# Optimization experiments

Hardware: AMD Instinct MI355X
Metric: run time of the kernel (lower is better)

The kernel has to match this reference:

```python
import jax, jax.numpy as jnp
import numpy as np

DIM_K = 32


def setup_inputs() -> dict:
    N, DORI, DAPP, DK, NCLS = 4096, 2048, 512, 32, 21
    key = jax.random.key(0)
    ks = jax.random.split(key, 16)
    std = 0.01
    inp = {
        'rois': jax.random.normal(ks[0], (N, 5), jnp.float32),
        'delta_rois': jax.random.normal(ks[1], (9, N, 5), jnp.float32),
        'features': jax.random.normal(ks[2], (9, N, DORI), jnp.float32),
        'gt_features': jax.random.normal(ks[3], (1, N, DORI), jnp.float32),
        'ious': jax.random.uniform(ks[4], (9, 1, N), jnp.float32),
        # learned parameters (singleton broadcast dims squeezed out)
        'attention_feat': jax.random.normal(ks[5], (DORI, DAPP), jnp.float32) * std,
        'w_k': jax.random.normal(ks[6], (DAPP, DK, 4), jnp.float32) * std,
        'w_q': jax.random.normal(ks[7], (9, DAPP, DK, 4), jnp.float32) * std,
        'alpha_w': jax.random.normal(ks[8], (9, DORI, 4), jnp.float32) * std,
        'bbox_regress': jax.random.normal(ks[9], (9, DORI, 4), jnp.float32) * 0.001,
        'w_k_cls': jax.random.normal(ks[10], (DAPP, DK, 1), jnp.float32) * std,
        'w_q_cls': jax.random.normal(ks[11], (9, DAPP, DK, 1), jnp.float32) * std,
        'alpha_w_cls': jax.random.normal(ks[12], (9, DORI, 1), jnp.float32) * std,
        'cls_score_w': jax.random.normal(ks[13], (9, DORI, NCLS), jnp.float32) * std,
    }
    return inp


def reference(rois, delta_rois, features, gt_features, ious,
              attention_feat, w_k, w_q, alpha_w, bbox_regress,
              w_k_cls, w_q_cls, alpha_w_cls, cls_score_w):
    # features: (9, N, DORI). The torch code materializes (9,N,DORI,DAPP)
    # via broadcast-mul + sum; einsum computes the identical contraction.
    off = jax.nn.relu(jnp.einsum('anf,fd->and', features, attention_feat))  # (9,N,DAPP)

    alpha = jnp.einsum('anf,afc->anc', features, alpha_w)          # (9,N,4)
    offset = jnp.einsum('anf,afc->anc', features, bbox_regress)   # (9,N,4)
    alpha_softmax = jax.nn.softmax(alpha, axis=0)
    delta8 = delta_rois[:, :, 1:5]                                  # (9,N,4)
    delta_pred_offset = delta8 + offset
    output = jnp.sum(delta_pred_offset * alpha_softmax, axis=0)    # (N,4)

    # ---- classification branch ----
    cls_score = jnp.einsum('anf,afc->anc', features, cls_score_w)  # (9,N,NCLS)
    alpha_cls = jnp.einsum('anf,afc->anc', features, alpha_w_cls)  # (9,N,1)
    alpha_softmax_cls = jax.nn.softmax(alpha_cls, axis=0)

    # ---- training-only beta (query/key) attention ----
    query_out = jnp.einsum('and,adkc->ankc', off, w_q)          # (9,N,DK,4)
    query_out_cls = jnp.einsum('and,adkc->ankc', off, w_q_cls)  # (9,N,DK,1)
    gt_off = jax.nn.relu(jnp.einsum('nf,fd->nd', gt_features[0], attention_feat))  # (N,DAPP)
    key_out = jnp.einsum('nd,dkc->nkc', gt_off, w_k)            # (N,DK,4)
    key_out_cls = jnp.einsum('nd,dkc->nkc', gt_off, w_k_cls)    # (N,DK,1)

    scale = 1.0 / np.sqrt(DIM_K).astype(np.float32)
    beta_out = jnp.einsum('ankc,nkc->anc', query_out, key_out) * scale - ious[:, 0, :, None]  # (9,N,4)
    beta_softmax = jax.nn.softmax(beta_out, axis=0)
    beta_out_cls = jnp.einsum('ankc,nkc->anc', query_out_cls, key_out_cls) * scale - ious.reshape(9, -1, 1)  # (9,N,1)
    beta_softmax_cls = jax.nn.softmax(beta_out_cls, axis=0)

    output_beta = jnp.sum(delta_pred_offset * beta_softmax, axis=0)  # (N,4)

    return (output, output_beta, alpha_softmax, beta_softmax,
            delta_pred_offset, delta_pred_offset, alpha, beta_out,
            cls_score, alpha_softmax_cls, beta_softmax_cls, alpha_cls, beta_out_cls)
```

## Files before the change

### kernel.cpp

```cpp
#include <hip/hip_runtime.h>

using u16 = unsigned short;
using s16x8 = __attribute__((ext_vector_type(8))) short;
using f32x4 = __attribute__((ext_vector_type(4))) float;

#define DEVI __device__ __forceinline__

constexpr int AN = 9, NB = 10, NN = 4096, DORI = 2048, DAPP = 512, NCLS = 21, QCOLS = 160;

constexpr size_t O0 = 0;
constexpr size_t O1 = 16384;
constexpr size_t O2 = 32768;
constexpr size_t O3 = 180224;
constexpr size_t O4 = 327680;
constexpr size_t O5 = 475136;
constexpr size_t O6 = 622592;
constexpr size_t O7 = 770048;
constexpr size_t O8 = 917504;
constexpr size_t O9 = 1691648;
constexpr size_t O10 = 1728512;
constexpr size_t O11 = 1765376;
constexpr size_t O12 = 1802240;

DEVI u16 f2b(float f) {
  unsigned u = __float_as_uint(f);
  unsigned r = (u + 0x7fffu + ((u >> 16) & 1u)) >> 16;
  return (u16)r;
}

DEVI uint4 pack8(float4 u, float4 v) {
  uint4 r;
  r.x = (unsigned)f2b(u.x) | ((unsigned)f2b(u.y) << 16);
  r.y = (unsigned)f2b(u.z) | ((unsigned)f2b(u.w) << 16);
  r.z = (unsigned)f2b(v.x) | ((unsigned)f2b(v.y) << 16);
  r.w = (unsigned)f2b(v.z) | ((unsigned)f2b(v.w) << 16);
  return r;
}

DEVI void gload_lds16(const u16* g, u16* l) {
  __builtin_amdgcn_global_load_lds(
      (const __attribute__((address_space(1))) void*)g,
      (__attribute__((address_space(3))) void*)l, 16, 0, 0);
}

__global__ __launch_bounds__(256) void prep(const float* __restrict__ att,
                                            const float* __restrict__ wq,
                                            const float* __restrict__ wqc,
                                            const float* __restrict__ wk,
                                            const float* __restrict__ wkc,
                                            const float* __restrict__ aw,
                                            const float* __restrict__ bb,
                                            const float* __restrict__ awc,
                                            const float* __restrict__ cw,
                                            const float* __restrict__ gt,
                                            u16* __restrict__ attB,
                                            u16* __restrict__ Wq,
                                            u16* __restrict__ Wsm,
                                            u16* __restrict__ featB9) {
  const int b = blockIdx.x, tid = threadIdx.x;
  if (b < 4096) {
    int t = b * 256 + tid;
    int c = t / DORI, d = t % DORI;
    attB[t] = f2b(att[(size_t)d * DAPP + c]);
  } else if (b < 7296) {
    int t = (b - 4096) * 256 + tid;
    int bq = t / (QCOLS * DAPP);
    int r = t % (QCOLS * DAPP);
    int col = r / DAPP, d = r % DAPP;
    float v;
    if (bq < 9) {
      if (col < 128) v = wq[(size_t)bq * DAPP * 128 + (size_t)d * 128 + col];
      else           v = wqc[(size_t)bq * DAPP * 32 + (size_t)d * 32 + (col - 128)];
    } else {
      if (col < 128) v = wk[(size_t)d * 128 + col];
      else           v = wkc[(size_t)d * 32 + (col - 128)];
    }
    Wq[t] = f2b(v);
  } else if (b < 7368) {
    int t = (b - 7296) * 256 + tid;
    if (t >= AN * DORI) return;
    int a = t / DORI, f = t % DORI;
    u16* Wa = Wsm + (size_t)a * 32 * DORI;
    for (int c = 0; c < 4; ++c)  Wa[c * DORI + f]       = f2b(aw[((size_t)a * DORI + f) * 4 + c]);
    for (int c = 0; c < 4; ++c)  Wa[(4 + c) * DORI + f] = f2b(bb[((size_t)a * DORI + f) * 4 + c]);
    for (int c = 0; c < 21; ++c) Wa[(8 + c) * DORI + f] = f2b(cw[((size_t)a * DORI + f) * 21 + c]);
    Wa[29 * DORI + f] = f2b(awc[(size_t)a * DORI + f]);
    Wa[30 * DORI + f] = 0;
    Wa[31 * DORI + f] = 0;
  } else {
    if (!featB9) return;
    long i = (long)(b - 7368) * 256 + tid;
    float4 v0 = ((const float4*)gt)[i * 2];
    float4 v1 = ((const float4*)gt)[i * 2 + 1];
    ((uint4*)featB9)[i] = pack8(v0, v1);
  }
}

__global__ __launch_bounds__(256) void feat_gemm(const float* __restrict__ feat,
                                                 const u16* __restrict__ Wsm,
                                                 float* __restrict__ smallf,
                                                 u16* __restrict__ wb,
                                                 float* __restrict__ cls_out) {
  __shared__ __align__(16) u16 As[64 * 32];
  __shared__ __align__(16) u16 Bs[32 * 32];
  const int tid = threadIdx.x, lane = tid & 63, wave = tid >> 6;
  const int tileM = blockIdx.y * 64, batch = blockIdx.z;
  const float* Ab = feat + ((size_t)batch * NN + tileM) * DORI;
  const u16* Bb = Wsm + (size_t)batch * 32 * DORI;
  u16* wbp = wb ? wb + ((size_t)batch * NN + tileM) * DORI : nullptr;

  f32x4 acc0 = {0.f, 0.f, 0.f, 0.f}, acc1 = {0.f, 0.f, 0.f, 0.f};
  const int arow = tid >> 2, acol = (tid & 3) * 8;
  const bool bact = tid < 128;

  uint4 raA, rbA, raB, rbB;
  auto loadA = [&](int k0) {
    const float* s = Ab + (size_t)arow * DORI + k0 + acol;
    raA = pack8(*(const float4*)s, *(const float4*)(s + 4));
    if (bact) rbA = *(const uint4*)(Bb + (size_t)arow * DORI + k0 + acol);
  };
  auto loadB = [&](int k0) {
    const float* s = Ab + (size_t)arow * DORI + k0 + acol;
    raB = pack8(*(const float4*)s, *(const float4*)(s + 4));
    if (bact) rbB = *(const uint4*)(Bb + (size_t)arow * DORI + k0 + acol);
  };
  loadA(0);
  loadB(32);
  const u16* Arow = As + (wave * 16 + (lane & 15)) * 32 + (lane >> 4) * 8;
  const u16* Brow = Bs + (lane & 15) * 32 + (lane >> 4) * 8;

  for (int k0 = 0; k0 < DORI; k0 += 64) {
    __syncthreads();
    *(uint4*)(As + (size_t)tid * 8) = raA;
    if (bact) *(uint4*)(Bs + (size_t)tid * 8) = rbA;
    if (wbp) *(uint4*)(wbp + (size_t)arow * DORI + k0 + acol) = raA;
    __syncthreads();
    if (k0 + 64 < DORI) loadA(k0 + 64);
    {
      s16x8 af = *(const s16x8*)Arow;
      s16x8 b0 = *(const s16x8*)Brow;
      s16x8 b1 = *(const s16x8*)(Brow + 16 * 32);
      acc0 = __builtin_amdgcn_mfma_f32_16x16x32_bf16(af, b0, acc0, 0, 0, 0);
      acc1 = __builtin_amdgcn_mfma_f32_16x16x32_bf16(af, b1, acc1, 0, 0, 0);
    }
    __syncthreads();
    *(uint4*)(As + (size_t)tid * 8) = raB;
    if (bact) *(uint4*)(Bs + (size_t)tid * 8) = rbB;
    if (wbp) *(uint4*)(wbp + (size_t)arow * DORI + k0 + 32 + acol) = raB;
    __syncthreads();
    if (k0 + 96 < DORI) loadB(k0 + 96);
    {
      s16x8 af = *(const s16x8*)Arow;
      s16x8 b0 = *(const s16x8*)Brow;
      s16x8 b1 = *(const s16x8*)(Brow + 16 * 32);
      acc0 = __builtin_amdgcn_mfma_f32_16x16x32_bf16(af, b0, acc0, 0, 0, 0);
      acc1 = __builtin_amdgcn_mfma_f32_16x16x32_bf16(af, b1, acc1, 0, 0, 0);
    }
  }

  const int r0 = tileM + wave * 16 + (lane >> 4) * 4;
  const int c0 = lane & 15;
#pragma unroll
  for (int q = 0; q < 4; ++q) {
    const size_t an = (size_t)batch * NN + r0 + q;
    smallf[an * 32 + c0]      = acc0[q];
    smallf[an * 32 + c0 + 16] = acc1[q];
    if (c0 >= 8)  cls_out[an * 21 + (c0 - 8)] = acc0[q];
    if (c0 <= 12) cls_out[an * 21 + (c0 + 8)] = acc1[q];
  }
}

template<int BM, int BN, int WM, int WN, bool RELU, bool OUTBF, bool SWZ>
__global__ __launch_bounds__(WM * WN * 64)
void gemm_glds(const u16* __restrict__ A, long sA, const u16* __restrict__ B, long sB,
               void* __restrict__ Cv, long sC, int N, int K) {
  constexpr int THREADS = WM * WN * 64;
  constexpr int WTM = BM / WM, WTN = BN / WN;
  constexpr int FM = WTM / 16, FN = WTN / 16;
  constexpr int ACHN = BM * 4, BCHN = BN * 4;
  constexpr int ACH = (ACHN + THREADS - 1) / THREADS;
  constexpr int BCH = (BCHN + THREADS - 1) / THREADS;
  constexpr bool AFULL = (ACHN % THREADS) == 0, BFULL = (BCHN % THREADS) == 0;

  __shared__ __align__(16) u16 As[BM * 32];
  __shared__ __align__(16) u16 Bs[BN * 32];

  int bx = blockIdx.x, by = blockIdx.y, bz = blockIdx.z;
  if constexpr (SWZ) {
    int gx = gridDim.x, gy = gridDim.y;
    int h = bx + gx * (by + gy * bz);
    int nwg = gx * gy * (int)gridDim.z;
    int cpx = nwg >> 3;
    int l = (h & 7) * cpx + (h >> 3);
    bx = l % gx; l /= gx; by = l % gy; bz = l / gy;
  }

  const int tid = threadIdx.x, lane = tid & 63, wave = tid >> 6;
  const int wm = wave % WM, wn = wave / WM;
  const int tileN = bx * BN, tileM = by * BM;
  const u16* Ab = A + (size_t)bz * sA + (size_t)tileM * K;
  const u16* Bb = B + (size_t)bz * sB + (size_t)tileN * K;

  f32x4 acc[FM][FN];
#pragma unroll
  for (int i = 0; i < FM; ++i)
#pragma unroll
    for (int j = 0; j < FN; ++j) acc[i][j] = (f32x4){0.f, 0.f, 0.f, 0.f};

  const u16* Arow = As + (wm * WTM + (lane & 15)) * 32 + (lane >> 4) * 8;
  const u16* Brow = Bs + (wn * WTN + (lane & 15)) * 32 + (lane >> 4) * 8;

  for (int k0 = 0; k0 < K; k0 += 32) {
#pragma unroll
    for (int i = 0; i < ACH; ++i) {
      int c = tid + i * THREADS;
      if (AFULL || c < ACHN)
        gload_lds16(Ab + (size_t)(c >> 2) * K + k0 + (c & 3) * 8, As + c * 8);
    }
#pragma unroll
    for (int i = 0; i < BCH; ++i) {
      int c = tid + i * THREADS;
      if (BFULL || c < BCHN)
        gload_lds16(Bb + (size_t)(c >> 2) * K + k0 + (c & 3) * 8, Bs + c * 8);
    }
    __syncthreads();
    s16x8 af[FM], bfr[FN];
#pragma unroll
    for (int i = 0; i < FM; ++i) af[i] = *(const s16x8*)(Arow + i * 16 * 32);
#pragma unroll
    for (int j = 0; j < FN; ++j) bfr[j] = *(const s16x8*)(Brow + j * 16 * 32);
#pragma unroll
    for (int i = 0; i < FM; ++i)
#pragma unroll
      for (int j = 0; j < FN; ++j)
        acc[i][j] = __builtin_amdgcn_mfma_f32_16x16x32_bf16(af[i], bfr[j], acc[i][j], 0, 0, 0);
    __syncthreads();
  }

  const int r0 = tileM + wm * WTM + (lane >> 4) * 4;
  const int c0 = tileN + wn * WTN + (lane & 15);
#pragma unroll
  for (int i = 0; i < FM; ++i)
#pragma unroll
    for (int j = 0; j < FN; ++j)
#pragma unroll
      for (int q = 0; q < 4; ++q) {
        float v = acc[i][j][q];
        if (RELU) v = fmaxf(v, 0.f);
        size_t idx = (size_t)bz * sC + (size_t)(r0 + i * 16 + q) * N + (c0 + j * 16);
        if (OUTBF) ((u16*)Cv)[idx] = f2b(v);
        else       ((float*)Cv)[idx] = v;
      }
}

template<int BM, int BN, int WM, int WN, bool RELU, bool OUTBF>
__global__ __launch_bounds__(WM * WN * 64)
void gemm_af32(const float* __restrict__ Av, const float* __restrict__ A2v, long sA,
               const u16* __restrict__ B, long sB,
               void* __restrict__ Cv, long sC, int N, int K) {
  constexpr int THREADS = WM * WN * 64;
  constexpr int WTM = BM / WM, WTN = BN / WN;
  constexpr int FM = WTM / 16, FN = WTN / 16;
  constexpr int ACH = (BM * 4) / THREADS;
  constexpr int BCHN = BN * 4;
  constexpr int BCH = (BCHN + THREADS - 1) / THREADS;
  constexpr bool BFULL = (BCHN % THREADS) == 0;

  __shared__ __align__(16) u16 As[BM * 32];
  __shared__ __align__(16) u16 Bs[BN * 32];

  const int tid = threadIdx.x, lane = tid & 63, wave = tid >> 6;
  const int wm = wave % WM, wn = wave / WM;
  const int tileN = blockIdx.x * BN, tileM = blockIdx.y * BM;
  const int batch = blockIdx.z;
  const float* base = (batch < 9) ? (Av + (size_t)batch * sA) : A2v;
  const float* Ab32 = base + (size_t)tileM * K;
  const u16* Bb = B + (size_t)batch * sB + (size_t)tileN * K;

  f32x4 acc[FM][FN];
#pragma unroll
  for (int i = 0; i < FM; ++i)
#pragma unroll
    for (int j = 0; j < FN; ++j) acc[i][j] = (f32x4){0.f, 0.f, 0.f, 0.f};

  uint4 ra[ACH], rb[BCH];
  auto load_t = [&](int k0) {
#pragma unroll
    for (int i = 0; i < ACH; ++i) {
      int c = tid + i * THREADS;
      const float* s = Ab32 + (size_t)(c >> 2) * K + k0 + (c & 3) * 8;
      ra[i] = pack8(*(const float4*)s, *(const float4*)(s + 4));
    }
#pragma unroll
    for (int i = 0; i < BCH; ++i) {
      int c = tid + i * THREADS;
      if (BFULL || c < BCHN)
        rb[i] = *(const uint4*)(Bb + (size_t)(c >> 2) * K + k0 + (c & 3) * 8);
    }
  };

  load_t(0);
  const u16* Arow = As + (wm * WTM + (lane & 15)) * 32 + (lane >> 4) * 8;
  const u16* Brow = Bs + (wn * WTN + (lane & 15)) * 32 + (lane >> 4) * 8;

  for (int k0 = 0; k0 < K; k0 += 32) {
    __syncthreads();
#pragma unroll
    for (int i = 0; i < ACH; ++i)
      *(uint4*)(As + (size_t)(tid + i * THREADS) * 8) = ra[i];
#pragma unroll
    for (int i = 0; i < BCH; ++i) {
      int c = tid + i * THREADS;
      if (BFULL || c < BCHN) *(uint4*)(Bs + (size_t)c * 8) = rb[i];
    }
    __syncthreads();
    if (k0 + 32 < K) load_t(k0 + 32);
    s16x8 af[FM], bfr[FN];
#pragma unroll
    for (int i = 0; i < FM; ++i) af[i] = *(const s16x8*)(Arow + i * 16 * 32);
#pragma unroll
    for (int j = 0; j < FN; ++j) bfr[j] = *(const s16x8*)(Brow + j * 16 * 32);
#pragma unroll
    for (int i = 0; i < FM; ++i)
#pragma unroll
      for (int j = 0; j < FN; ++j)
        acc[i][j] = __builtin_amdgcn_mfma_f32_16x16x32_bf16(af[i], bfr[j], acc[i][j], 0, 0, 0);
  }

  const int r0 = tileM + wm * WTM + (lane >> 4) * 4;
  const int c0 = tileN + wn * WTN + (lane & 15);
#pragma unroll
  for (int i = 0; i < FM; ++i)
#pragma unroll
    for (int j = 0; j < FN; ++j)
#pragma unroll
      for (int q = 0; q < 4; ++q) {
        float v = acc[i][j][q];
        if (RELU) v = fmaxf(v, 0.f);
        size_t idx = (size_t)batch * sC + (size_t)(r0 + i * 16 + q) * N + (c0 + j * 16);
        if (OUTBF) ((u16*)Cv)[idx] = f2b(v);
        else       ((float*)Cv)[idx] = v;
      }
}

__global__ __launch_bounds__(256) void gemm2qb(const u16* __restrict__ offb,
                                               const u16* __restrict__ Wq,
                                               const float* __restrict__ keyf,
                                               const float* __restrict__ ious,
                                               float* __restrict__ betaf,
                                               float* __restrict__ betac) {
  constexpr int BM = 128, BN = 160;
  __shared__ __align__(16) u16 As[BM * 32];
  __shared__ __align__(16) u16 Bs[BN * 32];
  const int tid = threadIdx.x, lane = tid & 63, wave = tid >> 6;
  const int tileM = blockIdx.x * BM;
  const int a = blockIdx.y;
  const u16* Ab = offb + ((size_t)a * NN + tileM) * DAPP;
  const u16* Bb = Wq + (size_t)a * QCOLS * DAPP;

  f32x4 acc[2][10];
#pragma unroll
  for (int i = 0; i < 2; ++i)
#pragma unroll
    for (int j = 0; j < 10; ++j) acc[i][j] = (f32x4){0.f, 0.f, 0.f, 0.f};

  const u16* Arow = As + (wave * 32 + (lane & 15)) * 32 + (lane >> 4) * 8;
  const u16* Brow = Bs + (lane & 15) * 32 + (lane >> 4) * 8;

  for (int k0 = 0; k0 < DAPP; k0 += 32) {
#pragma unroll
    for (int i = 0; i < 2; ++i) {
      int c = tid + i * 256;
      gload_lds16(Ab + (size_t)(c >> 2) * DAPP + k0 + (c & 3) * 8, As + c * 8);
    }
#pragma unroll
    for (int i = 0; i < 3; ++i) {
      int c = tid + i * 256;
      if (c < 640)
        gload_lds16(Bb + (size_t)(c >> 2) * DAPP + k0 + (c & 3) * 8, Bs + c * 8);
    }
    __syncthreads();
    s16x8 af[2], bfr[10];
#pragma unroll
    for (int i = 0; i < 2; ++i) af[i] = *(const s16x8*)(Arow + i * 16 * 32);
#pragma unroll
    for (int j = 0; j < 10; ++j) bfr[j] = *(const s16x8*)(Brow + j * 16 * 32);
#pragma unroll
    for (int i = 0; i < 2; ++i)
#pragma unroll
      for (int j = 0; j < 10; ++j)
        acc[i][j] = __builtin_amdgcn_mfma_f32_16x16x32_bf16(af[i], bfr[j], acc[i][j], 0, 0, 0);
    __syncthreads();
  }

  const float scale = 0.17677669529663687f;
  const int cg = lane & 15;
#pragma unroll
  for (int i = 0; i < 2; ++i)
#pragma unroll
    for (int q = 0; q < 4; ++q) {
      const int row = tileM + wave * 32 + i * 16 + (lane >> 4) * 4 + q;
      const float* kr = keyf + (size_t)row * QCOLS;
      float m = 0.f;
#pragma unroll
      for (int j = 0; j < 8; ++j) m += acc[i][j][q] * kr[cg + j * 16];
      float cl = acc[i][8][q] * kr[128 + cg] + acc[i][9][q] * kr[144 + cg];
      m += __shfl_xor(m, 4); m += __shfl_xor(m, 8);
      cl += __shfl_xor(cl, 1); cl += __shfl_xor(cl, 2);
      cl += __shfl_xor(cl, 4); cl += __shfl_xor(cl, 8);
      const float iou = ious[(size_t)a * NN + row];
      if (cg < 4)  betaf[((size_t)a * NN + row) * 4 + (lane & 3)] = m * scale - iou;
      if (cg == 0) betac[(size_t)a * NN + row] = cl * scale - iou;
    }
}

__global__ __launch_bounds__(256) void finalize(const float* __restrict__ smallf,
                                                const float* __restrict__ beta_ws,
                                                const float* __restrict__ betac_ws,
                                                const float* __restrict__ delta_rois,
                                                float* __restrict__ out) {
  int n = blockIdx.x * blockDim.x + threadIdx.x;
  if (n >= NN) return;

  for (int c = 0; c < 4; ++c) {
    float al[9], be[9], dp[9];
    float mA = -1e30f, mB = -1e30f;
    for (int a = 0; a < 9; ++a) {
      size_t an = (size_t)a * NN + n;
      al[a] = smallf[an * 32 + c];
      float off_ = smallf[an * 32 + 4 + c];
      dp[a] = delta_rois[an * 5 + 1 + c] + off_;
      be[a] = beta_ws[an * 4 + c];
      mA = fmaxf(mA, al[a]); mB = fmaxf(mB, be[a]);
    }
    float eA[9], eB[9], sA = 0.f, sB = 0.f;
    for (int a = 0; a < 9; ++a) {
      eA[a] = expf(al[a] - mA); sA += eA[a];
      eB[a] = expf(be[a] - mB); sB += eB[a];
    }
    float rA = 1.f / sA, rB = 1.f / sB;
    float ov = 0.f, obv = 0.f;
    for (int a = 0; a < 9; ++a) {
      size_t an = (size_t)a * NN + n;
      float as_ = eA[a] * rA, bs_ = eB[a] * rB;
      out[O2 + an * 4 + c] = as_;
      out[O3 + an * 4 + c] = bs_;
      out[O4 + an * 4 + c] = dp[a];
      out[O5 + an * 4 + c] = dp[a];
      out[O6 + an * 4 + c] = al[a];
      out[O7 + an * 4 + c] = be[a];
      ov += dp[a] * as_; obv += dp[a] * bs_;
    }
    out[O0 + (size_t)n * 4 + c] = ov;
    out[O1 + (size_t)n * 4 + c] = obv;
  }

  float ac[9], bc[9];
  float mA = -1e30f, mB = -1e30f;
  for (int a = 0; a < 9; ++a) {
    size_t an = (size_t)a * NN + n;
    ac[a] = smallf[an * 32 + 29];
    bc[a] = betac_ws[an];
    mA = fmaxf(mA, ac[a]); mB = fmaxf(mB, bc[a]);
  }
  float eA[9], eB[9], sA = 0.f, sB = 0.f;
  for (int a = 0; a < 9; ++a) {
    eA[a] = expf(ac[a] - mA); sA += eA[a];
    eB[a] = expf(bc[a] - mB); sB += eB[a];
  }
  float rA = 1.f / sA, rB = 1.f / sB;
  for (int a = 0; a < 9; ++a) {
    size_t an = (size_t)a * NN + n;
    out[O9 + an]  = eA[a] * rA;
    out[O10 + an] = eB[a] * rB;
    out[O11 + an] = ac[a];
    out[O12 + an] = bc[a];
  }
}

extern "C" void kernel_launch(void* const* d_in, const int* in_sizes, int n_in,
                              void* d_out, int out_size, void* d_ws, size_t ws_size,
                              hipStream_t stream) {
  const float* delta_rois = (const float*)d_in[1];
  const float* features   = (const float*)d_in[2];
  const float* gt_features= (const float*)d_in[3];
  const float* ious       = (const float*)d_in[4];
  const float* att        = (const float*)d_in[5];
  const float* w_k        = (const float*)d_in[6];
  const float* w_q        = (const float*)d_in[7];
  const float* alpha_w    = (const float*)d_in[8];
  const float* bbox       = (const float*)d_in[9];
  const float* w_k_cls    = (const float*)d_in[10];
  const float* w_q_cls    = (const float*)d_in[11];
  const float* alpha_w_cls= (const float*)d_in[12];
  const float* cls_w      = (const float*)d_in[13];
  float* out = (float*)d_out;

  char* ws = (char*)d_ws;
  u16* attB    = (u16*)ws;   ws += (size_t)DAPP * DORI * 2;
  u16* Wq      = (u16*)ws;   ws += (size_t)NB * QCOLS * DAPP * 2;
  u16* Wsmall  = (u16*)ws;   ws += (size_t)AN * 32 * DORI * 2;
  u16* offb    = (u16*)ws;   ws += (size_t)NB * NN * DAPP * 2;
  float* smallf= (float*)ws; ws += (size_t)AN * NN * 32 * 4;
  float* keyf  = (float*)ws; ws += (size_t)NN * QCOLS * 4;
  float* betaf = (float*)ws; ws += (size_t)AN * NN * 4 * 4;
  float* betac = (float*)ws; ws += (size_t)AN * NN * 4;
  size_t base_bytes = (size_t)(ws - (char*)d_ws);
  size_t featB_bytes = (size_t)NB * NN * DORI * 2;
  bool big = ws_size >= base_bytes + featB_bytes;
  u16* featB = big ? (u16*)ws : nullptr;

  prep<<<11464, 256, 0, stream>>>(att, w_q, w_q_cls, w_k, w_k_cls, alpha_w, bbox,
                                  alpha_w_cls, cls_w, gt_features, attB, Wq, Wsmall,
                                  big ? featB + (size_t)AN * NN * DORI : nullptr);

  dim3 gf(1, NN / 64, AN);
  feat_gemm<<<gf, 256, 0, stream>>>(features, Wsmall, smallf, featB, out + O8);

  dim3 g1(DAPP / 128, NN / 128, NB);
  if (big) {
    gemm_glds<128, 128, 2, 2, true, true, true><<<g1, 256, 0, stream>>>(
        featB, (long)NN * DORI, attB, 0, offb, (long)NN * DAPP, DAPP, DORI);
  } else {
    gemm_af32<128, 128, 2, 2, true, true><<<g1, 256, 0, stream>>>(
        features, gt_features, (long)NN * DORI, attB, 0, offb, (long)NN * DAPP, DAPP, DORI);
  }

  dim3 gk(QCOLS / 32, NN / 128, 1);
  gemm_glds<128, 32, 4, 1, false, false, false><<<gk, 256, 0, stream>>>(
      offb + (size_t)9 * NN * DAPP, 0, Wq + (size_t)9 * QCOLS * DAPP, 0,
      keyf, 0, QCOLS, DAPP);

  dim3 g2(NN / 128, AN, 1);
  gemm2qb<<<g2, 256, 0, stream>>>(offb, Wq, keyf, ious, betaf, betac);

  finalize<<<NN / 256, 256, 0, stream>>>(smallf, betaf, betac, delta_rois, out);
}
```

Before: 340.1 us.

## Fuse small-weight GEMM and attention-feature GEMM into one kernel reading fp32 features once

Replaces the separate feat_gemm (which wrote a bf16 copy of features) and the big feature×attention GEMM with a single 512-thread kernel. Each block loads a 64-row fp32 feature tile once, converts it to bf16, and multiplies it against all 512 attention columns plus the 32 small-weight columns. The aim is to avoid writing and re-reading a bf16 copy of the features and to drop a launch. In exchange the M tile is only 64 rows, the grid is small at 640 blocks, the B tile in LDS is large, and the k-loop has no LDS double buffering.

```diff
diff --git a/kernel.cpp b/kernel.cpp
--- a/kernel.cpp
+++ b/kernel.cpp
@@ -52,11 +52,9 @@
                                             const float* __restrict__ bb,
                                             const float* __restrict__ awc,
                                             const float* __restrict__ cw,
-                                            const float* __restrict__ gt,
                                             u16* __restrict__ attB,
                                             u16* __restrict__ Wq,
-                                            u16* __restrict__ Wsm,
-                                            u16* __restrict__ featB9) {
+                                            u16* __restrict__ Wsm) {
   const int b = blockIdx.x, tid = threadIdx.x;
   if (b < 4096) {
     int t = b * 256 + tid;
@@ -76,7 +74,7 @@
       else           v = wkc[(size_t)d * 32 + (col - 128)];
     }
     Wq[t] = f2b(v);
-  } else if (b < 7368) {
+  } else {
     int t = (b - 7296) * 256 + tid;
     if (t >= AN * DORI) return;
     int a = t / DORI, f = t % DORI;
@@ -87,86 +85,110 @@
     Wa[29 * DORI + f] = f2b(awc[(size_t)a * DORI + f]);
     Wa[30 * DORI + f] = 0;
     Wa[31 * DORI + f] = 0;
-  } else {
-    if (!featB9) return;
-    long i = (long)(b - 7368) * 256 + tid;
-    float4 v0 = ((const float4*)gt)[i * 2];
-    float4 v1 = ((const float4*)gt)[i * 2 + 1];
-    ((uint4*)featB9)[i] = pack8(v0, v1);
-  }
-}
-
-__global__ __launch_bounds__(256) void feat_gemm(const float* __restrict__ feat,
-                                                 const u16* __restrict__ Wsm,
-                                                 float* __restrict__ smallf,
-                                                 u16* __restrict__ wb,
-                                                 float* __restrict__ cls_out) {
+  }
+}
+
+__global__ __launch_bounds__(512) void mega(const float* __restrict__ feat,
+                                            const float* __restrict__ gt,
+                                            const u16* __restrict__ attB,
+                                            const u16* __restrict__ Wsm,
+                                            u16* __restrict__ offb,
+                                            float* __restrict__ smallf,
+                                            float* __restrict__ cls_out) {
   __shared__ __align__(16) u16 As[64 * 32];
-  __shared__ __align__(16) u16 Bs[32 * 32];
-  const int tid = threadIdx.x, lane = tid & 63, wave = tid >> 6;
-  const int tileM = blockIdx.y * 64, batch = blockIdx.z;
-  const float* Ab = feat + ((size_t)batch * NN + tileM) * DORI;
-  const u16* Bb = Wsm + (size_t)batch * 32 * DORI;
-  u16* wbp = wb ? wb + ((size_t)batch * NN + tileM) * DORI : nullptr;
-
-  f32x4 acc0 = {0.f, 0.f, 0.f, 0.f}, acc1 = {0.f, 0.f, 0.f, 0.f};
+  __shared__ __align__(16) u16 Bs[544 * 32];
+  const int tid = threadIdx.x, lane = tid & 63, w = tid >> 6;
+  const int tileM = blockIdx.y * 64, z = blockIdx.z;
+  const float* Ab = ((z < 9) ? feat + (size_t)z * NN * DORI : gt) + (size_t)tileM * DORI;
+  const u16* Wb = Wsm + (size_t)((z < 9) ? z : 0) * 32 * DORI;
+
+  f32x4 acc[4][4], accS[4];
+#pragma unroll
+  for (int i = 0; i < 4; ++i) {
+#pragma unroll
+    for (int j = 0; j < 4; ++j) acc[i][j] = (f32x4){0.f, 0.f, 0.f, 0.f};
+    accS[i] = (f32x4){0.f, 0.f, 0.f, 0.f};
+  }
+
   const int arow = tid >> 2, acol = (tid & 3) * 8;
-  const bool bact = tid < 128;
-
-  uint4 raA, rbA, raB, rbB;
-  auto loadA = [&](int k0) {
+  const bool aact = tid < 256;
+  uint4 raA, raB;
+  auto loadA = [&](int k0, uint4& r) {
     const float* s = Ab + (size_t)arow * DORI + k0 + acol;
-    raA = pack8(*(const float4*)s, *(const float4*)(s + 4));
-    if (bact) rbA = *(const uint4*)(Bb + (size_t)arow * DORI + k0 + acol);
+    r = pack8(*(const float4*)s, *(const float4*)(s + 4));
   };
-  auto loadB = [&](int k0) {
-    const float* s = Ab + (size_t)arow * DORI + k0 + acol;
-    raB = pack8(*(const float4*)s, *(const float4*)(s + 4));
-    if (bact) rbB = *(const uint4*)(Bb + (size_t)arow * DORI + k0 + acol);
+  if (aact) { loadA(0, raA); loadA(32, raB); }
+
+  auto stageB = [&](int k0) {
+#pragma unroll
+    for (int i = 0; i < 4; ++i) {
+      int c = tid + i * 512;
+      gload_lds16(attB + (size_t)(c >> 2) * DORI + k0 + (c & 3) * 8, Bs + c * 8);
+    }
+    if (tid < 128) {
+      int c = 2048 + tid;
+      gload_lds16(Wb + (size_t)((c >> 2) - 512) * DORI + k0 + (c & 3) * 8, Bs + c * 8);
+    }
   };
-  loadA(0);
-  loadB(32);
-  const u16* Arow = As + (wave * 16 + (lane & 15)) * 32 + (lane >> 4) * 8;
-  const u16* Brow = Bs + (lane & 15) * 32 + (lane >> 4) * 8;
+
+  const u16* Arow = As + (lane & 15) * 32 + (lane >> 4) * 8;
+  const u16* Brow = Bs + (w * 64 + (lane & 15)) * 32 + (lane >> 4) * 8;
+  const u16* BrowS = Bs + (512 + w * 16 + (lane & 15)) * 32 + (lane >> 4) * 8;
+
+  auto step = [&](int k0, uint4 ra) {
+    if (aact) *(uint4*)(As + (size_t)tid * 8) = ra;
+    stageB(k0);
+    __syncthreads();
+    s16x8 af[4], bfr[4];
+#pragma unroll
+    for (int i = 0; i < 4; ++i) af[i] = *(const s16x8*)(Arow + i * 16 * 32);
+#pragma unroll
+    for (int j = 0; j < 4; ++j) bfr[j] = *(const s16x8*)(Brow + j * 16 * 32);
+#pragma unroll
+    for (int i = 0; i < 4; ++i)
+#pragma unroll
+      for (int j = 0; j < 4; ++j)
+        acc[i][j] = __builtin_amdgcn_mfma_f32_16x16x32_bf16(af[i], bfr[j], acc[i][j], 0, 0, 0);
+    if (w < 2) {
+      s16x8 bs = *(const s16x8*)BrowS;
+#pragma unroll
+      for (int i = 0; i < 4; ++i)
+        accS[i] = __builtin_amdgcn_mfma_f32_16x16x32_bf16(af[i], bs, accS[i], 0, 0, 0);
+    }
+    __syncthreads();
+  };
 
   for (int k0 = 0; k0 < DORI; k0 += 64) {
-    __syncthreads();
-    *(uint4*)(As + (size_t)tid * 8) = raA;
-    if (bact) *(uint4*)(Bs + (size_t)tid * 8) = rbA;
-    if (wbp) *(uint4*)(wbp + (size_t)arow * DORI + k0 + acol) = raA;
-    __syncthreads();
-    if (k0 + 64 < DORI) loadA(k0 + 64);
-    {
-      s16x8 af = *(const s16x8*)Arow;
-      s16x8 b0 = *(const s16x8*)Brow;
-      s16x8 b1 = *(const s16x8*)(Brow + 16 * 32);
-      acc0 = __builtin_amdgcn_mfma_f32_16x16x32_bf16(af, b0, acc0, 0, 0, 0);
-      acc1 = __builtin_amdgcn_mfma_f32_16x16x32_bf16(af, b1, acc1, 0, 0, 0);
-    }
-    __syncthreads();
-    *(uint4*)(As + (size_t)tid * 8) = raB;
-    if (bact) *(uint4*)(Bs + (size_t)tid * 8) = rbB;
-    if (wbp) *(uint4*)(wbp + (size_t)arow * DORI + k0 + 32 + acol) = raB;
-    __syncthreads();
-    if (k0 + 96 < DORI) loadB(k0 + 96);
-    {
-      s16x8 af = *(const s16x8*)Arow;
-      s16x8 b0 = *(const s16x8*)Brow;
-      s16x8 b1 = *(const s16x8*)(Brow + 16 * 32);
-      acc0 = __builtin_amdgcn_mfma_f32_16x16x32_bf16(af, b0, acc0, 0, 0, 0);
-      acc1 = __builtin_amdgcn_mfma_f32_16x16x32_bf16(af, b1, acc1, 0, 0, 0);
-    }
-  }
-
-  const int r0 = tileM + wave * 16 + (lane >> 4) * 4;
-  const int c0 = lane & 15;
-#pragma unroll
-  for (int q = 0; q < 4; ++q) {
-    const size_t an = (size_t)batch * NN + r0 + q;
-    smallf[an * 32 + c0]      = acc0[q];
-    smallf[an * 32 + c0 + 16] = acc1[q];
-    if (c0 >= 8)  cls_out[an * 21 + (c0 - 8)] = acc0[q];
-    if (c0 <= 12) cls_out[an * 21 + (c0 + 8)] = acc1[q];
+    uint4 curA = raA, curB = raB;
+    if (aact && k0 + 64 < DORI) loadA(k0 + 64, raA);
+    step(k0, curA);
+    if (aact && k0 + 96 < DORI) loadA(k0 + 96, raB);
+    step(k0 + 32, curB);
+  }
+
+#pragma unroll
+  for (int i = 0; i < 4; ++i) {
+    const int row = tileM + i * 16 + (lane >> 4) * 4;
+    const int col = w * 64 + (lane & 15);
+#pragma unroll
+    for (int j = 0; j < 4; ++j)
+#pragma unroll
+      for (int q = 0; q < 4; ++q)
+        offb[((size_t)z * NN + row + q) * DAPP + col + j * 16] =
+            f2b(fmaxf(acc[i][j][q], 0.f));
+  }
+  if (w < 2 && z < 9) {
+    const int cs = w * 16 + (lane & 15);
+#pragma unroll
+    for (int i = 0; i < 4; ++i) {
+      const int row = tileM + i * 16 + (lane >> 4) * 4;
+#pragma unroll
+      for (int q = 0; q < 4; ++q) {
+        const size_t an = (size_t)z * NN + row + q;
+        smallf[an * 32 + cs] = accS[i][q];
+        if (cs >= 8 && cs <= 28) cls_out[an * 21 + (cs - 8)] = accS[i][q];
+      }
+    }
   }
 }
 
@@ -248,96 +270,6 @@
         float v = acc[i][j][q];
         if (RELU) v = fmaxf(v, 0.f);
         size_t idx = (size_t)bz * sC + (size_t)(r0 + i * 16 + q) * N + (c0 + j * 16);
-        if (OUTBF) ((u16*)Cv)[idx] = f2b(v);
-        else       ((float*)Cv)[idx] = v;
-      }
-}
-
-template<int BM, int BN, int WM, int WN, bool RELU, bool OUTBF>
-__global__ __launch_bounds__(WM * WN * 64)
-void gemm_af32(const float* __restrict__ Av, const float* __restrict__ A2v, long sA,
-               const u16* __restrict__ B, long sB,
-               void* __restrict__ Cv, long sC, int N, int K) {
-  constexpr int THREADS = WM * WN * 64;
-  constexpr int WTM = BM / WM, WTN = BN / WN;
-  constexpr int FM = WTM / 16, FN = WTN / 16;
-  constexpr int ACH = (BM * 4) / THREADS;
-  constexpr int BCHN = BN * 4;
-  constexpr int BCH = (BCHN + THREADS - 1) / THREADS;
-  constexpr bool BFULL = (BCHN % THREADS) == 0;
-
-  __shared__ __align__(16) u16 As[BM * 32];
-  __shared__ __align__(16) u16 Bs[BN * 32];
-
-  const int tid = threadIdx.x, lane = tid & 63, wave = tid >> 6;
-  const int wm = wave % WM, wn = wave / WM;
-  const int tileN = blockIdx.x * BN, tileM = blockIdx.y * BM;
-  const int batch = blockIdx.z;
-  const float* base = (batch < 9) ? (Av + (size_t)batch * sA) : A2v;
-  const float* Ab32 = base + (size_t)tileM * K;
-  const u16* Bb = B + (size_t)batch * sB + (size_t)tileN * K;
-
-  f32x4 acc[FM][FN];
-#pragma unroll
-  for (int i = 0; i < FM; ++i)
-#pragma unroll
-    for (int j = 0; j < FN; ++j) acc[i][j] = (f32x4){0.f, 0.f, 0.f, 0.f};
-
-  uint4 ra[ACH], rb[BCH];
-  auto load_t = [&](int k0) {
-#pragma unroll
-    for (int i = 0; i < ACH; ++i) {
-      int c = tid + i * THREADS;
-      const float* s = Ab32 + (size_t)(c >> 2) * K + k0 + (c & 3) * 8;
-      ra[i] = pack8(*(const float4*)s, *(const float4*)(s + 4));
-    }
-#pragma unroll
-    for (int i = 0; i < BCH; ++i) {
-      int c = tid + i * THREADS;
-      if (BFULL || c < BCHN)
-        rb[i] = *(const uint4*)(Bb + (size_t)(c >> 2) * K + k0 + (c & 3) * 8);
-    }
-  };
-
-  load_t(0);
-  const u16* Arow = As + (wm * WTM + (lane & 15)) * 32 + (lane >> 4) * 8;
-  const u16* Brow = Bs + (wn * WTN + (lane & 15)) * 32 + (lane >> 4) * 8;
-
-  for (int k0 = 0; k0 < K; k0 += 32) {
-    __syncthreads();
-#pragma unroll
-    for (int i = 0; i < ACH; ++i)
-      *(uint4*)(As + (size_t)(tid + i * THREADS) * 8) = ra[i];
-#pragma unroll
-    for (int i = 0; i < BCH; ++i) {
-      int c = tid + i * THREADS;
-      if (BFULL || c < BCHN) *(uint4*)(Bs + (size_t)c * 8) = rb[i];
-    }
-    __syncthreads();
-    if (k0 + 32 < K) load_t(k0 + 32);
-    s16x8 af[FM], bfr[FN];
-#pragma unroll
-    for (int i = 0; i < FM; ++i) af[i] = *(const s16x8*)(Arow + i * 16 * 32);
-#pragma unroll
-    for (int j = 0; j < FN; ++j) bfr[j] = *(const s16x8*)(Brow + j * 16 * 32);
-#pragma unroll
-    for (int i = 0; i < FM; ++i)
-#pragma unroll
-      for (int j = 0; j < FN; ++j)
-        acc[i][j] = __builtin_amdgcn_mfma_f32_16x16x32_bf16(af[i], bfr[j], acc[i][j], 0, 0, 0);
-  }
-
-  const int r0 = tileM + wm * WTM + (lane >> 4) * 4;
-  const int c0 = tileN + wn * WTN + (lane & 15);
-#pragma unroll
-  for (int i = 0; i < FM; ++i)
-#pragma unroll
-    for (int j = 0; j < FN; ++j)
-#pragma unroll
-      for (int q = 0; q < 4; ++q) {
-        float v = acc[i][j][q];
-        if (RELU) v = fmaxf(v, 0.f);
-        size_t idx = (size_t)batch * sC + (size_t)(r0 + i * 16 + q) * N + (c0 + j * 16);
         if (OUTBF) ((u16*)Cv)[idx] = f2b(v);
         else       ((float*)Cv)[idx] = v;
       }
@@ -505,26 +437,13 @@
   float* keyf  = (float*)ws; ws += (size_t)NN * QCOLS * 4;
   float* betaf = (float*)ws; ws += (size_t)AN * NN * 4 * 4;
   float* betac = (float*)ws; ws += (size_t)AN * NN * 4;
-  size_t base_bytes = (size_t)(ws - (char*)d_ws);
-  size_t featB_bytes = (size_t)NB * NN * DORI * 2;
-  bool big = ws_size >= base_bytes + featB_bytes;
-  u16* featB = big ? (u16*)ws : nullptr;
-
-  prep<<<11464, 256, 0, stream>>>(att, w_q, w_q_cls, w_k, w_k_cls, alpha_w, bbox,
-                                  alpha_w_cls, cls_w, gt_features, attB, Wq, Wsmall,
-                                  big ? featB + (size_t)AN * NN * DORI : nullptr);
-
-  dim3 gf(1, NN / 64, AN);
-  feat_gemm<<<gf, 256, 0, stream>>>(features, Wsmall, smallf, featB, out + O8);
-
-  dim3 g1(DAPP / 128, NN / 128, NB);
-  if (big) {
-    gemm_glds<128, 128, 2, 2, true, true, true><<<g1, 256, 0, stream>>>(
-        featB, (long)NN * DORI, attB, 0, offb, (long)NN * DAPP, DAPP, DORI);
-  } else {
-    gemm_af32<128, 128, 2, 2, true, true><<<g1, 256, 0, stream>>>(
-        features, gt_features, (long)NN * DORI, attB, 0, offb, (long)NN * DAPP, DAPP, DORI);
-  }
+
+  prep<<<7368, 256, 0, stream>>>(att, w_q, w_q_cls, w_k, w_k_cls, alpha_w, bbox,
+                                 alpha_w_cls, cls_w, attB, Wq, Wsmall);
+
+  dim3 gm(1, NN / 64, NB);
+  mega<<<gm, 512, 0, stream>>>(features, gt_features, attB, Wsmall,
+                               offb, smallf, out + O8);
 
   dim3 gk(QCOLS / 32, NN / 128, 1);
   gemm_glds<128, 32, 4, 1, false, false, false><<<gk, 256, 0, stream>>>(
```

Result: slower. 358.6 us (+5.5%).

## Split fused feature cast+small GEMM into standalone cast and LDS-direct small GEMM

Applied to the files above, without the earlier changes.

Replaces the feat_gemm kernel, which converted fp32 features to bf16 while also writing the bf16 copy and computing the small alpha/offset/cls projections, with a separate grid-stride cast kernel and a new gemm_small kernel. gemm_small reads the bf16 copy through global_load_lds with 128-row tiles. The aim is to stop the small, MFMA-light GEMM from being bound by the fp32 loads and conversion. In exchange the bf16 features (about 150MB) are re-read once more. The fallback path now uses gemm_af32 plus a cls_copy kernel.

```diff
diff --git a/kernel.cpp b/kernel.cpp
--- a/kernel.cpp
+++ b/kernel.cpp
@@ -41,6 +41,17 @@
   __builtin_amdgcn_global_load_lds(
       (const __attribute__((address_space(1))) void*)g,
       (__attribute__((address_space(3))) void*)l, 16, 0, 0);
+}
+
+__global__ __launch_bounds__(256) void cast_kernel(const float* __restrict__ src,
+                                                   u16* __restrict__ dst, long n8) {
+  long i = (long)blockIdx.x * blockDim.x + threadIdx.x;
+  long stride = (long)gridDim.x * blockDim.x;
+  for (; i < n8; i += stride) {
+    float4 v0 = ((const float4*)src)[i * 2];
+    float4 v1 = ((const float4*)src)[i * 2 + 1];
+    ((uint4*)dst)[i] = pack8(v0, v1);
+  }
 }
 
 __global__ __launch_bounds__(256) void prep(const float* __restrict__ att,
@@ -96,80 +107,6 @@
   }
 }
 
-__global__ __launch_bounds__(256) void feat_gemm(const float* __restrict__ feat,
-                                                 const u16* __restrict__ Wsm,
-                                                 float* __restrict__ smallf,
-                                                 u16* __restrict__ wb,
-                                                 float* __restrict__ cls_out) {
-  __shared__ __align__(16) u16 As[64 * 32];
-  __shared__ __align__(16) u16 Bs[32 * 32];
-  const int tid = threadIdx.x, lane = tid & 63, wave = tid >> 6;
-  const int tileM = blockIdx.y * 64, batch = blockIdx.z;
-  const float* Ab = feat + ((size_t)batch * NN + tileM) * DORI;
-  const u16* Bb = Wsm + (size_t)batch * 32 * DORI;
-  u16* wbp = wb ? wb + ((size_t)batch * NN + tileM) * DORI : nullptr;
-
-  f32x4 acc0 = {0.f, 0.f, 0.f, 0.f}, acc1 = {0.f, 0.f, 0.f, 0.f};
-  const int arow = tid >> 2, acol = (tid & 3) * 8;
-  const bool bact = tid < 128;
-
-  uint4 raA, rbA, raB, rbB;
-  auto loadA = [&](int k0) {
-    const float* s = Ab + (size_t)arow * DORI + k0 + acol;
-    raA = pack8(*(const float4*)s, *(const float4*)(s + 4));
-    if (bact) rbA = *(const uint4*)(Bb + (size_t)arow * DORI + k0 + acol);
-  };
-  auto loadB = [&](int k0) {
-    const float* s = Ab + (size_t)arow * DORI + k0 + acol;
-    raB = pack8(*(const float4*)s, *(const float4*)(s + 4));
-    if (bact) rbB = *(const uint4*)(Bb + (size_t)arow * DORI + k0 + acol);
-  };
-  loadA(0);
-  loadB(32);
-  const u16* Arow = As + (wave * 16 + (lane & 15)) * 32 + (lane >> 4) * 8;
-  const u16* Brow = Bs + (lane & 15) * 32 + (lane >> 4) * 8;
-
-  for (int k0 = 0; k0 < DORI; k0 += 64) {
-    __syncthreads();
-    *(uint4*)(As + (size_t)tid * 8) = raA;
-    if (bact) *(uint4*)(Bs + (size_t)tid * 8) = rbA;
-    if (wbp) *(uint4*)(wbp + (size_t)arow * DORI + k0 + acol) = raA;
-    __syncthreads();
-    if (k0 + 64 < DORI) loadA(k0 + 64);
-    {
-      s16x8 af = *(const s16x8*)Arow;
-      s16x8 b0 = *(const s16x8*)Brow;
-      s16x8 b1 = *(const s16x8*)(Brow + 16 * 32);
-      acc0 = __builtin_amdgcn_mfma_f32_16x16x32_bf16(af, b0, acc0, 0, 0, 0);
-      acc1 = __builtin_amdgcn_mfma_f32_16x16x32_bf16(af, b1, acc1, 0, 0, 0);
-    }
-    __syncthreads();
-    *(uint4*)(As + (size_t)tid * 8) = raB;
-    if (bact) *(uint4*)(Bs + (size_t)tid * 8) = rbB;
-    if (wbp) *(uint4*)(wbp + (size_t)arow * DORI + k0 + 32 + acol) = raB;
-    __syncthreads();
-    if (k0 + 96 < DORI) loadB(k0 + 96);
-    {
-      s16x8 af = *(const s16x8*)Arow;
-      s16x8 b0 = *(const s16x8*)Brow;
-      s16x8 b1 = *(const s16x8*)(Brow + 16 * 32);
-      acc0 = __builtin_amdgcn_mfma_f32_16x16x32_bf16(af, b0, acc0, 0, 0, 0);
-      acc1 = __builtin_amdgcn_mfma_f32_16x16x32_bf16(af, b1, acc1, 0, 0, 0);
-    }
-  }
-
-  const int r0 = tileM + wave * 16 + (lane >> 4) * 4;
-  const int c0 = lane & 15;
-#pragma unroll
-  for (int q = 0; q < 4; ++q) {
-    const size_t an = (size_t)batch * NN + r0 + q;
-    smallf[an * 32 + c0]      = acc0[q];
-    smallf[an * 32 + c0 + 16] = acc1[q];
-    if (c0 >= 8)  cls_out[an * 21 + (c0 - 8)] = acc0[q];
-    if (c0 <= 12) cls_out[an * 21 + (c0 + 8)] = acc1[q];
-  }
-}
-
 template<int BM, int BN, int WM, int WN, bool RELU, bool OUTBF, bool SWZ>
 __global__ __launch_bounds__(WM * WN * 64)
 void gemm_glds(const u16* __restrict__ A, long sA, const u16* __restrict__ B, long sB,
@@ -250,6 +187,63 @@
         size_t idx = (size_t)bz * sC + (size_t)(r0 + i * 16 + q) * N + (c0 + j * 16);
         if (OUTBF) ((u16*)Cv)[idx] = f2b(v);
         else       ((float*)Cv)[idx] = v;
+      }
+}
+
+__global__ __launch_bounds__(256) void gemm_small(const u16* __restrict__ A,
+                                                  const u16* __restrict__ Wsm,
+                                                  float* __restrict__ smallf,
+                                                  float* __restrict__ cls_out) {
+  __shared__ __align__(16) u16 As[128 * 32];
+  __shared__ __align__(16) u16 Bs[32 * 32];
+  const int tid = threadIdx.x, lane = tid & 63, wave = tid >> 6;
+  const int tileM = blockIdx.y * 128, bz = blockIdx.z;
+  const u16* Ab = A + ((size_t)bz * NN + tileM) * DORI;
+  const u16* Bb = Wsm + (size_t)bz * 32 * DORI;
+
+  f32x4 acc[2][2];
+#pragma unroll
+  for (int i = 0; i < 2; ++i)
+#pragma unroll
+    for (int j = 0; j < 2; ++j) acc[i][j] = (f32x4){0.f, 0.f, 0.f, 0.f};
+
+  const u16* Arow = As + (wave * 32 + (lane & 15)) * 32 + (lane >> 4) * 8;
+  const u16* Brow = Bs + (lane & 15) * 32 + (lane >> 4) * 8;
+
+  for (int k0 = 0; k0 < DORI; k0 += 32) {
+#pragma unroll
+    for (int i = 0; i < 2; ++i) {
+      int c = tid + i * 256;
+      gload_lds16(Ab + (size_t)(c >> 2) * DORI + k0 + (c & 3) * 8, As + c * 8);
+    }
+    if (tid < 128)
+      gload_lds16(Bb + (size_t)(tid >> 2) * DORI + k0 + (tid & 3) * 8, Bs + tid * 8);
+    __syncthreads();
+    s16x8 af[2], bfr[2];
+#pragma unroll
+    for (int i = 0; i < 2; ++i) af[i] = *(const s16x8*)(Arow + i * 16 * 32);
+#pragma unroll
+    for (int j = 0; j < 2; ++j) bfr[j] = *(const s16x8*)(Brow + j * 16 * 32);
+#pragma unroll
+    for (int i = 0; i < 2; ++i)
+#pragma unroll
+      for (int j = 0; j < 2; ++j)
+        acc[i][j] = __builtin_amdgcn_mfma_f32_16x16x32_bf16(af[i], bfr[j], acc[i][j], 0, 0, 0);
+    __syncthreads();
+  }
+
+#pragma unroll
+  for (int i = 0; i < 2; ++i)
+#pragma unroll
+    for (int j = 0; j < 2; ++j)
+#pragma unroll
+      for (int q = 0; q < 4; ++q) {
+        const int row = tileM + wave * 32 + i * 16 + (lane >> 4) * 4 + q;
+        const int col = j * 16 + (lane & 15);
+        const size_t an = (size_t)bz * NN + row;
+        float v = acc[i][j][q];
+        smallf[an * 32 + col] = v;
+        if (col >= 8 && col <= 28) cls_out[an * 21 + (col - 8)] = v;
       }
 }
 
@@ -341,6 +335,14 @@
         if (OUTBF) ((u16*)Cv)[idx] = f2b(v);
         else       ((float*)Cv)[idx] = v;
       }
+}
+
+__global__ __launch_bounds__(256) void cls_copy(const float* __restrict__ smallf,
+                                                float* __restrict__ o) {
+  int i = blockIdx.x * blockDim.x + threadIdx.x;
+  if (i >= AN * NN * NCLS) return;
+  int an = i / NCLS, c = i % NCLS;
+  o[i] = smallf[(size_t)an * 32 + 8 + c];
 }
 
 __global__ __launch_bounds__(256) void gemm2qb(const u16* __restrict__ offb,
@@ -514,16 +516,24 @@
                                   alpha_w_cls, cls_w, gt_features, attB, Wq, Wsmall,
                                   big ? featB + (size_t)AN * NN * DORI : nullptr);
 
-  dim3 gf(1, NN / 64, AN);
-  feat_gemm<<<gf, 256, 0, stream>>>(features, Wsmall, smallf, featB, out + O8);
-
-  dim3 g1(DAPP / 128, NN / 128, NB);
   if (big) {
+    cast_kernel<<<2048, 256, 0, stream>>>(features, featB, (long)AN * NN * DORI / 8);
+
+    dim3 gsm(1, NN / 128, AN);
+    gemm_small<<<gsm, 256, 0, stream>>>(featB, Wsmall, smallf, out + O8);
+
+    dim3 g1(DAPP / 128, NN / 128, NB);
     gemm_glds<128, 128, 2, 2, true, true, true><<<g1, 256, 0, stream>>>(
         featB, (long)NN * DORI, attB, 0, offb, (long)NN * DAPP, DAPP, DORI);
   } else {
+    dim3 g1(DAPP / 128, NN / 128, NB);
     gemm_af32<128, 128, 2, 2, true, true><<<g1, 256, 0, stream>>>(
         features, gt_features, (long)NN * DORI, attB, 0, offb, (long)NN * DAPP, DAPP, DORI);
+    dim3 gsm(1, NN / 128, AN);
+    gemm_af32<128, 32, 4, 1, false, false><<<gsm, 256, 0, stream>>>(
+        features, nullptr, (long)NN * DORI, Wsmall, (long)32 * DORI,
+        smallf, (long)NN * 32, 32, DORI);
+    cls_copy<<<(AN * NN * NCLS + 255) / 256, 256, 0, stream>>>(smallf, out + O8);
   }
 
   dim3 gk(QCOLS / 32, NN / 128, 1);
```

After: 348.1 us. +2.4%, slower.
